# Kernel optimization log

Measured on AMD Instinct MI355X. Metric: run time of the kernel, lower is better.

The kernel has to match this reference:

```python
import jax, jax.numpy as jnp
import numpy as np

D_MODEL = 1024
N_HEADS = 16
HEAD = D_MODEL // N_HEADS
B, T = 4, 2048


def setup_inputs() -> dict:
    key = jax.random.key(0)
    ks = jax.random.split(key, 8)
    s = 0.02
    return {
        "x_enc": jax.random.normal(ks[0], (B, T, D_MODEL), dtype=jnp.float32),
        "x_dec": jax.random.normal(ks[1], (B, T, D_MODEL), dtype=jnp.float32),
        "mask": jnp.zeros((B, T, T), dtype=jnp.float32),
        "Wq": jax.random.normal(ks[2], (D_MODEL, D_MODEL), dtype=jnp.float32) * s,
        "bq": jnp.zeros((D_MODEL,), dtype=jnp.float32),
        "Wkv": jax.random.normal(ks[3], (D_MODEL, 2 * D_MODEL), dtype=jnp.float32) * s,
        "bkv": jnp.zeros((2 * D_MODEL,), dtype=jnp.float32),
        "Wo": jax.random.normal(ks[4], (D_MODEL, D_MODEL), dtype=jnp.float32) * s,
        "bo": jnp.zeros((D_MODEL,), dtype=jnp.float32),
    }


def reference(x_enc, x_dec, mask, Wq, bq, Wkv, bkv, Wo, bo):
    b, t, c = x_enc.shape
    # projections
    kv = x_enc @ Wkv + bkv                     # [B,T,2C]
    q = x_dec @ Wq + bq                        # [B,T,C]
    # split heads (replicates torch reshape of interleaved kv)
    kv = kv.reshape(b, t, N_HEADS, 2 * HEAD).transpose(0, 2, 1, 3)  # [B,H,T,2hs]
    q = q.reshape(b, t, N_HEADS, HEAD).transpose(0, 2, 1, 3)        # [B,H,T,hs]
    k, v = kv[..., :HEAD], kv[..., HEAD:]
    # attention
    scores = jnp.einsum("bhqd,bhkd->bhqk", q, k) / np.sqrt(HEAD).astype(np.float32)
    scores = scores + mask[:, None, :, :]      # additive mask, broadcast over heads
    attn = jax.nn.softmax(scores, axis=-1)
    res = jnp.einsum("bhqk,bhkd->bhqd", attn, v)   # [B,H,T,hs]
    res = res.transpose(0, 2, 1, 3).reshape(b, t, c)
    return res @ Wo + bo
```

## Files before the change

### kernel.cpp

```cpp
#include <hip/hip_runtime.h>
#include <hip/hip_bf16.h>
#include <math.h>


#define D_MODEL 1024
#define NH      16
#define HEAD    64
#define BATCH   4
#define SEQ     2048
#define QB      256

#define LOG2E   1.44269504088896f

typedef unsigned int   u32;
typedef unsigned short u16;
typedef __attribute__((ext_vector_type(8))) short s16x8;
typedef __attribute__((ext_vector_type(4))) float f32x4;
typedef __attribute__((ext_vector_type(4))) unsigned int u32v4;

__device__ __forceinline__ u16 tobf(float f) {
    u32 u = __builtin_bit_cast(u32, f);
    return (u16)((u + 0x7fffu + ((u >> 16) & 1u)) >> 16);
}
__device__ __forceinline__ float frombf(u16 u) {
    return __builtin_bit_cast(float, (u32)u << 16);
}
__device__ __forceinline__ u32 cvtpk(float a, float b) {
    u32 r;
    asm("v_cvt_pk_bf16_f32 %0, %1, %2" : "=v"(r) : "v"(a), "v"(b));
    return r;
}
__device__ __forceinline__ float fexp2(float x) {
    float r;
    asm("v_exp_f32 %0, %1" : "=v"(r) : "v"(x));
    return r;
}

__device__ __forceinline__ void gl_lds16(const void* g, void* l) {
    __builtin_amdgcn_global_load_lds(
        (const __attribute__((address_space(1))) u32*)g,
        (__attribute__((address_space(3))) u32*)l, 16, 0, 0);
}

__global__ __launch_bounds__(256) void cast_bf16(
    const float* __restrict__ in, u16* __restrict__ out, int n)
{
    int i = (blockIdx.x * 256 + threadIdx.x) * 4;
    if (i < n) {
        float4 v = *(const float4*)(in + i);
        ushort4 o = make_ushort4(tobf(v.x), tobf(v.y), tobf(v.z), tobf(v.w));
        *(ushort4*)(out + i) = o;
    }
}

__global__ __launch_bounds__(256) void mask_prep(
    const float* __restrict__ mask, u16* __restrict__ mp)
{
    const size_t gt = (size_t)blockIdx.x * 256 + threadIdx.x;
    const int l = (int)(gt & 63);
    const size_t tile = gt >> 6;
    const int kt = (int)(tile & 127);
    const size_t bq = tile >> 7;
    const int qt = (int)(bq & 127);
    const int b  = (int)(bq >> 7);
    const int q15 = l & 15, quad = l >> 4;
    const int q = qt*16 + q15;
    const int k = (kt >> 2)*64 + ((kt >> 1) & 1)*32 + (kt & 1)*4 + quad*8;
    float4 v = *(const float4*)&mask[((size_t)(b*SEQ + q))*SEQ + k];
    ushort4 o = make_ushort4(tobf(v.x * LOG2E), tobf(v.y * LOG2E),
                             tobf(v.z * LOG2E), tobf(v.w * LOG2E));
    *(ushort4*)&mp[tile*256 + (size_t)l*4] = o;
}

__global__ __launch_bounds__(256) void transpose_cast(
    const float* __restrict__ W, u16* __restrict__ WT, int K, int N)
{
    __shared__ __align__(16) float tile[32][33];
    const int n0 = blockIdx.x * 32, k0 = blockIdx.y * 32;
    const int r = threadIdx.x >> 3, c4 = (threadIdx.x & 7) * 4;
    float4 v = *(const float4*)&W[(size_t)(k0 + r) * N + n0 + c4];
    tile[r][c4] = v.x; tile[r][c4+1] = v.y; tile[r][c4+2] = v.z; tile[r][c4+3] = v.w;
    __syncthreads();
    ushort4 o = make_ushort4(tobf(tile[c4+0][r]), tobf(tile[c4+1][r]),
                             tobf(tile[c4+2][r]), tobf(tile[c4+3][r]));
    *(ushort4*)&WT[(size_t)(n0 + r) * K + k0 + c4] = o;
}

__device__ __forceinline__ void store_out(u16* p, float v)  { *p = tobf(v); }
__device__ __forceinline__ void store_out(float* p, float v){ *p = v; }

template <typename OT>
__global__ __launch_bounds__(256) void gemm_bt(
    const u16* __restrict__ A, const u16* __restrict__ Bt,
    const float* __restrict__ bias, OT* __restrict__ C,
    int N, int K, float out_scale)
{
    __shared__ __align__(16) u16 As[2][128 * 32];
    __shared__ __align__(16) u16 Bs[2][128 * 32];
    const int t = threadIdx.x;
    const int w = t >> 6, l = t & 63;
    const int lane15 = l & 15, quad = l >> 4;
    const int m0 = blockIdx.y * 128, n0 = blockIdx.x * 128;
    const int wm = (w >> 1) * 64, wn = (w & 1) * 64;
    const int lr = l >> 2, lk = (l & 3) * 8;

    auto stage = [&](int k0, int bufi) {
        #pragma unroll
        for (int i = 0; i < 2; ++i) {
            const int chunk = w * 2 + i;
            gl_lds16(A  + (size_t)(m0 + chunk*16 + lr) * K + k0 + lk,
                     &As[bufi][chunk * 512]);
            gl_lds16(Bt + (size_t)(n0 + chunk*16 + lr) * K + k0 + lk,
                     &Bs[bufi][chunk * 512]);
        }
    };

    f32x4 acc[4][4] = {};
    const int nb = K >> 5;
    stage(0, 0);

    for (int i = 0; i < nb; ++i) {
        const int cur = i & 1;
        __syncthreads();
        if (i + 1 < nb) stage((i + 1) << 5, cur ^ 1);
        s16x8 af[4], bfr[4];
        #pragma unroll
        for (int i2 = 0; i2 < 4; ++i2)
            af[i2] = *(const s16x8*)&As[cur][(wm + i2*16 + lane15) * 32 + quad * 8];
        #pragma unroll
        for (int j = 0; j < 4; ++j)
            bfr[j] = *(const s16x8*)&Bs[cur][(wn + j*16 + lane15) * 32 + quad * 8];
        #pragma unroll
        for (int i2 = 0; i2 < 4; ++i2)
            #pragma unroll
            for (int j = 0; j < 4; ++j)
                acc[i2][j] = __builtin_amdgcn_mfma_f32_16x16x32_bf16(
                    af[i2], bfr[j], acc[i2][j], 0, 0, 0);
    }
    #pragma unroll
    for (int j = 0; j < 4; ++j) {
        const int col = n0 + wn + j*16 + lane15;
        const float bv = bias[col];
        #pragma unroll
        for (int i = 0; i < 4; ++i)
            #pragma unroll
            for (int r = 0; r < 4; ++r) {
                const int row = m0 + wm + i*16 + quad*4 + r;
                store_out(C + (size_t)row * N + col, (acc[i][j][r] + bv) * out_scale);
            }
    }
}

__global__ __launch_bounds__(256) void gemm_kv(
    const u16* __restrict__ A, const u16* __restrict__ Bt,
    const float* __restrict__ bias, u16* __restrict__ kvb,
    u16* __restrict__ vtb)
{
    const int N = 2 * D_MODEL, K = D_MODEL;
    __shared__ __align__(16) u16 As[2][128 * 32];
    __shared__ __align__(16) u16 Bs[2][128 * 32];
    const int t = threadIdx.x;
    const int w = t >> 6, l = t & 63;
    const int lane15 = l & 15, quad = l >> 4;
    const int m0 = blockIdx.y * 128, n0 = blockIdx.x * 128;
    const int wm = (w >> 1) * 64, wn = (w & 1) * 64;
    const int lr = l >> 2, lk = (l & 3) * 8;

    auto stage = [&](int k0, int bufi) {
        #pragma unroll
        for (int i = 0; i < 2; ++i) {
            const int chunk = w * 2 + i;
            gl_lds16(A  + (size_t)(m0 + chunk*16 + lr) * K + k0 + lk,
                     &As[bufi][chunk * 512]);
            gl_lds16(Bt + (size_t)(n0 + chunk*16 + lr) * K + k0 + lk,
                     &Bs[bufi][chunk * 512]);
        }
    };

    f32x4 acc[4][4] = {};
    const int nb = K >> 5;
    stage(0, 0);

    for (int i = 0; i < nb; ++i) {
        const int cur = i & 1;
        __syncthreads();
        if (i + 1 < nb) stage((i + 1) << 5, cur ^ 1);
        s16x8 af[4], bfr[4];
        #pragma unroll
        for (int i2 = 0; i2 < 4; ++i2)
            af[i2] = *(const s16x8*)&As[cur][(wm + i2*16 + lane15) * 32 + quad * 8];
        #pragma unroll
        for (int j = 0; j < 4; ++j)
            bfr[j] = *(const s16x8*)&Bs[cur][(wn + j*16 + lane15) * 32 + quad * 8];
        #pragma unroll
        for (int i2 = 0; i2 < 4; ++i2)
            #pragma unroll
            for (int j = 0; j < 4; ++j)
                acc[i2][j] = __builtin_amdgcn_mfma_f32_16x16x32_bf16(
                    af[i2], bfr[j], acc[i2][j], 0, 0, 0);
    }

    if (wn == 0) {
        #pragma unroll
        for (int j = 0; j < 4; ++j) {
            const int col = n0 + j*16 + lane15;
            const float bv = bias[col];
            #pragma unroll
            for (int i = 0; i < 4; ++i)
                #pragma unroll
                for (int r = 0; r < 4; ++r) {
                    const int row = m0 + wm + i*16 + quad*4 + r;
                    kvb[(size_t)row * N + col] = tobf(acc[i][j][r] + bv);
                }
        }
    } else {
        const int bh = (m0 >> 11) * NH + (n0 >> 7);
        #pragma unroll
        for (int j = 0; j < 4; ++j) {
            const int d = j*16 + lane15;
            const float bv = bias[n0 + 64 + d];
            #pragma unroll
            for (int i = 0; i < 4; ++i) {
                const int row = m0 + wm + i*16 + quad*4;
                const int tt = row & (SEQ - 1);
                u16* p = vtb + ((size_t)bh*64 + d)*SEQ + tt;
                *(uint2*)p = make_uint2(cvtpk(acc[i][j][0]+bv, acc[i][j][1]+bv),
                                        cvtpk(acc[i][j][2]+bv, acc[i][j][3]+bv));
            }
        }
    }
}

__global__ __launch_bounds__(512, 4) void attn_mfma(
    const u16* __restrict__ qb, const u16* __restrict__ kvb,
    const u16* __restrict__ vt, const u16* __restrict__ mp,
    u16* __restrict__ resb)
{
    __shared__ __align__(16) u16 sm[4*4096];
    const int t = threadIdx.x;
    const int w = t >> 6, l = t & 63;
    const int lane15 = l & 15, quad = l >> 4;
    const int h  = blockIdx.x;
    const int q0 = blockIdx.y * QB;
    const int b  = blockIdx.z;
    const int bh = b * NH + h;
    const int lr4 = l >> 2;
    const int lc8 = (((l & 3) ^ (lr4 & 3)) * 8);
    const int cq  = (quad ^ (lane15 & 3)) * 8;
    const int kprow = (lr4 >> 2)*8 + (lr4 & 3);

    s16x8 aq0[2], aq1[2];
    #pragma unroll
    for (int s = 0; s < 2; ++s) {
        const u16* qrow = qb + (size_t)(b*SEQ + q0 + w*32 + s*16 + lane15) * D_MODEL + h*HEAD;
        aq0[s] = *(const s16x8*)(qrow + quad*8);
        aq1[s] = *(const s16x8*)(qrow + 32 + quad*8);
    }
    const u16* mrow[2];
    #pragma unroll
    for (int s = 0; s < 2; ++s)
        mrow[s] = mp + (((size_t)b*128 + (q0>>4) + w*2 + s) * 128) * 256 + (size_t)l*4;

    auto stage = [&](int k0s, int bf) {
        const int hh = w & 1, rr = w >> 1;
        const int krow = (rr >> 1)*32 + (rr & 1)*4 + kprow;
        const u16* kg = kvb + (size_t)(b*SEQ + k0s + krow) * (2*D_MODEL)
                            + h*128 + hh*32 + lc8;
        gl_lds16(kg, sm + bf*4096 + hh*2048 + rr*512);
        const u16* vg = vt + (size_t)(bh*64 + rr*16 + lr4) * SEQ
                           + k0s + hh*32 + lc8;
        gl_lds16(vg, sm + 8192 + bf*4096 + hh*2048 + rr*512);
    };

    f32x4 o_acc[2][4] = {};
    f32x4 l_acc[2] = {};
    ushort4 mreg[2][4];
    s16x8 vones;
    #pragma unroll
    for (int i = 0; i < 8; ++i) vones[i] = (short)0x3F80;

    stage(0, 0);
    #pragma unroll
    for (int s = 0; s < 2; ++s)
        #pragma unroll
        for (int nt = 0; nt < 4; ++nt)
            mreg[s][nt] = *(const ushort4*)(mrow[s] + (size_t)nt * 256);

    for (int it = 0; it < SEQ/64; ++it) {
        const int k0 = it * 64;
        const int bf = it & 1;
        __syncthreads();
        if (it + 1 < SEQ/64)
            stage(k0 + 64, bf ^ 1);

        f32x4 sv[2][4];
        #pragma unroll
        for (int s = 0; s < 2; ++s)
            #pragma unroll
            for (int nt = 0; nt < 4; ++nt) {
                sv[s][nt][0] = frombf(mreg[s][nt].x); sv[s][nt][1] = frombf(mreg[s][nt].y);
                sv[s][nt][2] = frombf(mreg[s][nt].z); sv[s][nt][3] = frombf(mreg[s][nt].w);
            }
        __builtin_amdgcn_s_setprio(1);
        #pragma unroll
        for (int nt = 0; nt < 4; ++nt) {
            s16x8 kf0 = *(const s16x8*)(sm + bf*4096 +        (nt*16 + lane15)*32 + cq);
            s16x8 kf1 = *(const s16x8*)(sm + bf*4096 + 2048 + (nt*16 + lane15)*32 + cq);
            #pragma unroll
            for (int s = 0; s < 2; ++s) {
                sv[s][nt] = __builtin_amdgcn_mfma_f32_16x16x32_bf16(kf0, aq0[s], sv[s][nt], 0, 0, 0);
                sv[s][nt] = __builtin_amdgcn_mfma_f32_16x16x32_bf16(kf1, aq1[s], sv[s][nt], 0, 0, 0);
            }
        }
        __builtin_amdgcn_s_setprio(0);

        if (it + 1 < SEQ/64) {
            #pragma unroll
            for (int s = 0; s < 2; ++s)
                #pragma unroll
                for (int nt = 0; nt < 4; ++nt)
                    mreg[s][nt] = *(const ushort4*)(mrow[s] + ((size_t)((k0+64)>>4) + nt) * 256);
        }

        s16x8 pf[2][2];
        #pragma unroll
        for (int s = 0; s < 2; ++s)
            #pragma unroll
            for (int hf = 0; hf < 2; ++hf) {
                u32v4 pk;
                pk[0] = cvtpk(fexp2(sv[s][2*hf][0]),   fexp2(sv[s][2*hf][1]));
                pk[1] = cvtpk(fexp2(sv[s][2*hf][2]),   fexp2(sv[s][2*hf][3]));
                pk[2] = cvtpk(fexp2(sv[s][2*hf+1][0]), fexp2(sv[s][2*hf+1][1]));
                pk[3] = cvtpk(fexp2(sv[s][2*hf+1][2]), fexp2(sv[s][2*hf+1][3]));
                pf[s][hf] = __builtin_bit_cast(s16x8, pk);
            }

        __builtin_amdgcn_s_setprio(1);
        #pragma unroll
        for (int s = 0; s < 2; ++s) {
            l_acc[s] = __builtin_amdgcn_mfma_f32_16x16x32_bf16(vones, pf[s][0], l_acc[s], 0, 0, 0);
            l_acc[s] = __builtin_amdgcn_mfma_f32_16x16x32_bf16(vones, pf[s][1], l_acc[s], 0, 0, 0);
        }
        #pragma unroll
        for (int dt = 0; dt < 4; ++dt) {
            s16x8 vf0 = *(const s16x8*)(sm + 8192 + bf*4096 +        (dt*16 + lane15)*32 + cq);
            s16x8 vf1 = *(const s16x8*)(sm + 8192 + bf*4096 + 2048 + (dt*16 + lane15)*32 + cq);
            #pragma unroll
            for (int s = 0; s < 2; ++s) {
                o_acc[s][dt] = __builtin_amdgcn_mfma_f32_16x16x32_bf16(vf0, pf[s][0], o_acc[s][dt], 0, 0, 0);
                o_acc[s][dt] = __builtin_amdgcn_mfma_f32_16x16x32_bf16(vf1, pf[s][1], o_acc[s][dt], 0, 0, 0);
            }
        }
        __builtin_amdgcn_s_setprio(0);
    }

    __syncthreads();
    #pragma unroll
    for (int s = 0; s < 2; ++s) {
        const float inv = 1.f / l_acc[s][0];
        u16* orow = &sm[(w*32 + s*16 + lane15) * 64];
        #pragma unroll
        for (int dt = 0; dt < 4; ++dt) {
            *(uint2*)&orow[dt*16 + quad*4] = make_uint2(
                cvtpk(o_acc[s][dt][0]*inv, o_acc[s][dt][1]*inv),
                cvtpk(o_acc[s][dt][2]*inv, o_acc[s][dt][3]*inv));
        }
    }
    __syncthreads();
    {
        const int tr = t >> 1, tc = (t & 1) * 32;
        u16* o = resb + (size_t)(b*SEQ + q0 + tr) * D_MODEL + h*HEAD + tc;
        #pragma unroll
        for (int j = 0; j < 4; ++j)
            *(uint4*)(o + j*8) = *(const uint4*)&sm[tr*64 + tc + j*8];
    }
}

extern "C" void kernel_launch(void* const* d_in, const int* in_sizes, int n_in,
                              void* d_out, int out_size, void* d_ws, size_t ws_size,
                              hipStream_t stream) {
    const float* x_enc = (const float*)d_in[0];
    const float* x_dec = (const float*)d_in[1];
    const float* mask  = (const float*)d_in[2];
    const float* Wq    = (const float*)d_in[3];
    const float* bq    = (const float*)d_in[4];
    const float* Wkv   = (const float*)d_in[5];
    const float* bkv   = (const float*)d_in[6];
    const float* Wo    = (const float*)d_in[7];
    const float* bo    = (const float*)d_in[8];
    float* out = (float*)d_out;

    const int M = BATCH * SEQ;
    u16* xe   = (u16*)d_ws;
    u16* xd   = xe   + (size_t)M * D_MODEL;
    u16* wqT  = xd   + (size_t)M * D_MODEL;
    u16* wkvT = wqT  + (size_t)D_MODEL * D_MODEL;
    u16* woT  = wkvT + (size_t)2*D_MODEL*D_MODEL;
    u16* qbuf = woT  + (size_t)D_MODEL * D_MODEL;
    u16* kvb  = qbuf + (size_t)M * D_MODEL;
    u16* vtb  = kvb  + (size_t)M * 2 * D_MODEL;
    u16* resb = vtb  + (size_t)BATCH*NH*HEAD*SEQ;
    u16* mpk  = xe;

    const int NX = M * D_MODEL;
    cast_bf16<<<NX/1024, 256, 0, stream>>>(x_enc, xe, NX);
    cast_bf16<<<NX/1024, 256, 0, stream>>>(x_dec, xd, NX);
    transpose_cast<<<dim3(D_MODEL/32, D_MODEL/32), 256, 0, stream>>>(Wq,  wqT,  D_MODEL, D_MODEL);
    transpose_cast<<<dim3(2*D_MODEL/32, D_MODEL/32), 256, 0, stream>>>(Wkv, wkvT, D_MODEL, 2*D_MODEL);
    transpose_cast<<<dim3(D_MODEL/32, D_MODEL/32), 256, 0, stream>>>(Wo,  woT,  D_MODEL, D_MODEL);

    gemm_kv<<<dim3(2*D_MODEL/128, M/128), 256, 0, stream>>>(
        xe, wkvT, bkv, kvb, vtb);
    gemm_bt<u16><<<dim3(D_MODEL/128, M/128), 256, 0, stream>>>(
        xd, wqT, bq, qbuf, D_MODEL, D_MODEL, 0.125f * LOG2E);
    mask_prep<<<(BATCH*128*128*64)/256, 256, 0, stream>>>(mask, mpk);
    attn_mfma<<<dim3(NH, SEQ/QB, BATCH), 512, 0, stream>>>(
        qbuf, kvb, vtb, mpk, resb);
    gemm_bt<float><<<dim3(D_MODEL/128, M/128), 256, 0, stream>>>(
        resb, woT, bo, out, D_MODEL, D_MODEL, 1.0f);
}
```

Before: 384.4 us.

## Triple-buffer gemm_bt K loop and merge preprocessing launches

Changes the gemm_bt LDS staging from double to triple buffering, prefetching two K-steps ahead with a partial vmcnt wait, so global loads have more time to complete before they are consumed. It also merges the two input casts into one launch and the three weight transpose-casts into one launch, cutting launch overhead. Triple buffering raises LDS use per block, which may reduce occupancy. The custom waitcnt/barrier sequence depends on a fixed count of outstanding loads.

```diff
diff --git a/kernel.cpp b/kernel.cpp
--- a/kernel.cpp
+++ b/kernel.cpp
@@ -42,14 +42,17 @@
         (__attribute__((address_space(3))) u32*)l, 16, 0, 0);
 }
 
-__global__ __launch_bounds__(256) void cast_bf16(
-    const float* __restrict__ in, u16* __restrict__ out, int n)
-{
+__global__ __launch_bounds__(256) void cast_bf16_2(
+    const float* __restrict__ in0, const float* __restrict__ in1,
+    u16* __restrict__ out, int n)
+{
+    const float* in = blockIdx.y ? in1 : in0;
+    u16* o = out + (size_t)blockIdx.y * n;
     int i = (blockIdx.x * 256 + threadIdx.x) * 4;
     if (i < n) {
         float4 v = *(const float4*)(in + i);
-        ushort4 o = make_ushort4(tobf(v.x), tobf(v.y), tobf(v.z), tobf(v.w));
-        *(ushort4*)(out + i) = o;
+        ushort4 ov = make_ushort4(tobf(v.x), tobf(v.y), tobf(v.z), tobf(v.w));
+        *(ushort4*)(o + i) = ov;
     }
 }
 
@@ -72,11 +75,20 @@
     *(ushort4*)&mp[tile*256 + (size_t)l*4] = o;
 }
 
-__global__ __launch_bounds__(256) void transpose_cast(
-    const float* __restrict__ W, u16* __restrict__ WT, int K, int N)
-{
+__global__ __launch_bounds__(256) void transpose_cast4(
+    const float* __restrict__ Wq,  u16* __restrict__ wqT,
+    const float* __restrict__ Wkv, u16* __restrict__ wkvT,
+    const float* __restrict__ Wo,  u16* __restrict__ woT)
+{
+    const int K = D_MODEL;
+    const int z = blockIdx.z;
+    const float* W = (z == 0) ? Wq : (z == 3) ? Wo : Wkv;
+    u16* WT       = (z == 0) ? wqT : (z == 3) ? woT : wkvT;
+    const int N   = (z == 1 || z == 2) ? 2*D_MODEL : D_MODEL;
+    const int nb  = (z == 2) ? D_MODEL : 0;
+
     __shared__ __align__(16) float tile[32][33];
-    const int n0 = blockIdx.x * 32, k0 = blockIdx.y * 32;
+    const int n0 = nb + blockIdx.x * 32, k0 = blockIdx.y * 32;
     const int r = threadIdx.x >> 3, c4 = (threadIdx.x & 7) * 4;
     float4 v = *(const float4*)&W[(size_t)(k0 + r) * N + n0 + c4];
     tile[r][c4] = v.x; tile[r][c4+1] = v.y; tile[r][c4+2] = v.z; tile[r][c4+3] = v.w;
@@ -95,8 +107,8 @@
     const float* __restrict__ bias, OT* __restrict__ C,
     int N, int K, float out_scale)
 {
-    __shared__ __align__(16) u16 As[2][128 * 32];
-    __shared__ __align__(16) u16 Bs[2][128 * 32];
+    __shared__ __align__(16) u16 As[3][128 * 32];
+    __shared__ __align__(16) u16 Bs[3][128 * 32];
     const int t = threadIdx.x;
     const int w = t >> 6, l = t & 63;
     const int lane15 = l & 15, quad = l >> 4;
@@ -114,29 +126,43 @@
                      &Bs[bufi][chunk * 512]);
         }
     };
+    auto compute = [&](int cur, f32x4 (*acc)[4]) {
+        s16x8 af[4], bfr[4];
+        #pragma unroll
+        for (int i2 = 0; i2 < 4; ++i2)
+            af[i2] = *(const s16x8*)&As[cur][(wm + i2*16 + lane15) * 32 + quad * 8];
+        #pragma unroll
+        for (int j = 0; j < 4; ++j)
+            bfr[j] = *(const s16x8*)&Bs[cur][(wn + j*16 + lane15) * 32 + quad * 8];
+        #pragma unroll
+        for (int i2 = 0; i2 < 4; ++i2)
+            #pragma unroll
+            for (int j = 0; j < 4; ++j)
+                acc[i2][j] = __builtin_amdgcn_mfma_f32_16x16x32_bf16(
+                    af[i2], bfr[j], acc[i2][j], 0, 0, 0);
+    };
 
     f32x4 acc[4][4] = {};
     const int nb = K >> 5;
     stage(0, 0);
-
-    for (int i = 0; i < nb; ++i) {
-        const int cur = i & 1;
-        __syncthreads();
-        if (i + 1 < nb) stage((i + 1) << 5, cur ^ 1);
-        s16x8 af[4], bfr[4];
-        #pragma unroll
-        for (int i2 = 0; i2 < 4; ++i2)
-            af[i2] = *(const s16x8*)&As[cur][(wm + i2*16 + lane15) * 32 + quad * 8];
-        #pragma unroll
-        for (int j = 0; j < 4; ++j)
-            bfr[j] = *(const s16x8*)&Bs[cur][(wn + j*16 + lane15) * 32 + quad * 8];
-        #pragma unroll
-        for (int i2 = 0; i2 < 4; ++i2)
-            #pragma unroll
-            for (int j = 0; j < 4; ++j)
-                acc[i2][j] = __builtin_amdgcn_mfma_f32_16x16x32_bf16(
-                    af[i2], bfr[j], acc[i2][j], 0, 0, 0);
-    }
+    stage(32, 1);
+
+    for (int i = 0; i < nb - 1; ++i) {
+        const int cur = i % 3;
+        asm volatile("s_waitcnt vmcnt(4)" ::: "memory");
+        __builtin_amdgcn_sched_barrier(0);
+        __builtin_amdgcn_s_barrier();
+        if (i + 2 < nb) stage((i + 2) << 5, (i + 2) % 3);
+        compute(cur, acc);
+    }
+    {
+        const int cur = (nb - 1) % 3;
+        asm volatile("s_waitcnt vmcnt(0)" ::: "memory");
+        __builtin_amdgcn_sched_barrier(0);
+        __builtin_amdgcn_s_barrier();
+        compute(cur, acc);
+    }
+
     #pragma unroll
     for (int j = 0; j < 4; ++j) {
         const int col = n0 + wn + j*16 + lane15;
@@ -403,11 +429,9 @@
     u16* mpk  = xe;
 
     const int NX = M * D_MODEL;
-    cast_bf16<<<NX/1024, 256, 0, stream>>>(x_enc, xe, NX);
-    cast_bf16<<<NX/1024, 256, 0, stream>>>(x_dec, xd, NX);
-    transpose_cast<<<dim3(D_MODEL/32, D_MODEL/32), 256, 0, stream>>>(Wq,  wqT,  D_MODEL, D_MODEL);
-    transpose_cast<<<dim3(2*D_MODEL/32, D_MODEL/32), 256, 0, stream>>>(Wkv, wkvT, D_MODEL, 2*D_MODEL);
-    transpose_cast<<<dim3(D_MODEL/32, D_MODEL/32), 256, 0, stream>>>(Wo,  woT,  D_MODEL, D_MODEL);
+    cast_bf16_2<<<dim3(NX/1024, 2), 256, 0, stream>>>(x_enc, x_dec, xe, NX);
+    transpose_cast4<<<dim3(32, 32, 4), 256, 0, stream>>>(
+        Wq, wqT, Wkv, wkvT, Wo, woT);
 
     gemm_kv<<<dim3(2*D_MODEL/128, M/128), 256, 0, stream>>>(
         xe, wkvT, bkv, kvb, vtb);
```

New measurement: 382.3 us. No clear change (-0.5%).
